# Optimization experiments

Measured on AMD Instinct MI355X. Metric: run time of the kernel, lower is better.

Reference implementation:

```python
import jax, jax.numpy as jnp
import numpy as np

B, S, D, U = 32, 2048, 512, 512

def setup_inputs() -> dict:
    key = jax.random.key(0)
    k1, k2, k3, k4, k5 = jax.random.split(key, 5)
    passage = jax.random.normal(k1, (B, S, D), dtype=jnp.float32)
    hidden = jax.random.normal(k2, (B, D), dtype=jnp.float32)
    mask = jnp.ones((B, S), dtype=jnp.float32)
    # learned params (Dense kernels, glorot-ish scale)
    W1 = jax.random.normal(k3, (D, U), dtype=jnp.float32) / np.sqrt(D)
    W2 = jax.random.normal(k4, (D, U), dtype=jnp.float32) / np.sqrt(D)
    Vw = jax.random.normal(k5, (U, 1), dtype=jnp.float32) / np.sqrt(U)
    Vb = jnp.zeros((1,), dtype=jnp.float32)
    return {"passage": passage, "hidden": hidden, "mask": mask,
            "W1": W1, "W2": W2, "Vw": Vw, "Vb": Vb}

def reference(passage, hidden, mask, W1, W2, Vw, Vb):
    # passage: [B,S,D], hidden: [B,D], mask: [B,S]
    h_proj = jnp.einsum('bd,du->bu', hidden, W2)[:, None, :]        # [B,1,U]
    p_proj = jnp.einsum('bsd,du->bsu', passage, W1)                  # [B,S,U]
    score = jnp.einsum('bsu,uo->bso', jnp.tanh(p_proj + h_proj), Vw) + Vb  # [B,S,1]
    score = score + ((1.0 - mask) * -1e30)[:, :, None]
    attention_weights = jax.nn.softmax(score, axis=1)                # [B,S,1]
    context_vector = jnp.sum(attention_weights * passage, axis=1)    # [B,D]
    return context_vector, attention_weights
```

## Files before the change

### kernel.cpp

```cpp
#include <hip/hip_runtime.h>
#include <hip/hip_bf16.h>
#include <cstddef>


#define NB 32
#define NS 2048
#define ND 512
#define NU 512

typedef __bf16 bf16_t;
typedef __bf16 bf16x8 __attribute__((ext_vector_type(8)));
typedef float floatx4 __attribute__((ext_vector_type(4)));

__global__ __launch_bounds__(256) void prep_kernel(
    const float* __restrict__ W1, bf16_t* __restrict__ W1p,
    const float* __restrict__ hidden, const float* __restrict__ W2,
    float* __restrict__ hproj) {
    if (blockIdx.x < 128) {
        int wave = threadIdx.x >> 6, lane = threadIdx.x & 63;
        int f = (blockIdx.x << 2) + wave;
        int kc = f >> 5, ng = f & 31;
        int q = lane >> 4, c = lane & 15;
        const float* src = W1 + (kc * 32 + q * 8) * 512 + ng * 16 + c;
        bf16x8 w;
#pragma unroll
        for (int jj = 0; jj < 8; ++jj) w[jj] = (bf16_t)src[jj * 512];
        ((bf16x8*)W1p)[(f << 6) + lane] = w;
    } else {
        __shared__ float h[ND];
        __shared__ float part[256];
        int bi = blockIdx.x - 128;
        int b = bi >> 2, ug = bi & 3;
        int t = threadIdx.x;
        h[t] = hidden[b * ND + t];
        h[t + 256] = hidden[b * ND + t + 256];
        __syncthreads();
        int u = (ug << 7) + (t & 127);
        int d0 = (t >> 7) << 8;
        float acc = 0.f;
#pragma unroll 8
        for (int d = d0; d < d0 + 256; ++d) acc = fmaf(h[d], W2[d * NU + u], acc);
        part[t] = acc;
        __syncthreads();
        if (t < 128) hproj[b * NU + u] = part[t] + part[t + 128];
    }
}

__global__ __launch_bounds__(256)
__attribute__((amdgpu_waves_per_eu(2, 2)))
void score_kernel(
    const float* __restrict__ passage, const bf16_t* __restrict__ W1p,
    const float* __restrict__ hproj, const float* __restrict__ Vw,
    const float* __restrict__ Vb, float* __restrict__ scores) {
    __shared__ bf16_t As[64 * 512];
    __shared__ float red[4 * 64];
    const int tid = threadIdx.x;
    const int wave = tid >> 6, lane = tid & 63;
    const int q = lane >> 4, c = lane & 15;
    const int bid = blockIdx.x;
    const int mblk = ((bid >> 4) << 3) + (bid & 7);
    const int nhalf = (bid >> 3) & 1;
    const int m0 = mblk * 64;
    const int b = m0 >> 11;
    const int ng0 = (nhalf << 4) + (wave << 2);
    const bf16x8* Wq = (const bf16x8*)W1p;

#pragma unroll 4
    for (int cc = 0; cc < 16; ++cc) {
        int row = (cc << 2) + wave;
        const float* g = passage + ((size_t)(m0 + row) << 9) + (lane << 3);
        floatx4 f0 = *(const floatx4*)g;
        floatx4 f1 = *(const floatx4*)(g + 4);
        bf16x8 v;
        v[0] = (bf16_t)f0[0]; v[1] = (bf16_t)f0[1];
        v[2] = (bf16_t)f0[2]; v[3] = (bf16_t)f0[3];
        v[4] = (bf16_t)f1[0]; v[5] = (bf16_t)f1[1];
        v[6] = (bf16_t)f1[2]; v[7] = (bf16_t)f1[3];
        unsigned kb = (unsigned)(lane << 4) ^ (unsigned)((row & 7) << 4);
        *(bf16x8*)((char*)As + row * 1024 + kb) = v;
    }

    bf16x8 b_cur[4], b_nxt[4];
#pragma unroll
    for (int j = 0; j < 4; ++j)
        b_cur[j] = Wq[((ng0 + j) << 6) + lane];

    __syncthreads();

    floatx4 acc[4][4];
#pragma unroll
    for (int i = 0; i < 4; ++i)
#pragma unroll
        for (int j = 0; j < 4; ++j) { floatx4 z = {0.f, 0.f, 0.f, 0.f}; acc[i][j] = z; }

    bf16x8 a_cur[4], a_nxt[4];
#pragma unroll
    for (int i = 0; i < 4; ++i) {
        int row = (i << 4) + c;
        unsigned kb = (unsigned)(q << 4) ^ (unsigned)((row & 7) << 4);
        a_cur[i] = *(const bf16x8*)((const char*)As + row * 1024 + kb);
    }

#pragma unroll 2
    for (int kc = 0; kc < 16; ++kc) {
        if (kc < 15) {
#pragma unroll
            for (int j = 0; j < 4; ++j)
                b_nxt[j] = Wq[((((kc + 1) << 5) + ng0 + j) << 6) + lane];
#pragma unroll
            for (int i = 0; i < 4; ++i) {
                int row = (i << 4) + c;
                unsigned kb = (unsigned)(((kc + 1) << 6) + (q << 4)) ^ (unsigned)((row & 7) << 4);
                a_nxt[i] = *(const bf16x8*)((const char*)As + row * 1024 + kb);
            }
        }
        __builtin_amdgcn_s_setprio(1);
#pragma unroll
        for (int i = 0; i < 4; ++i)
#pragma unroll
            for (int j = 0; j < 4; ++j)
                acc[i][j] = __builtin_amdgcn_mfma_f32_16x16x32_bf16(a_cur[i], b_cur[j], acc[i][j], 0, 0, 0);
        __builtin_amdgcn_s_setprio(0);
#pragma unroll
        for (int i = 0; i < 4; ++i) a_cur[i] = a_nxt[i];
#pragma unroll
        for (int j = 0; j < 4; ++j) b_cur[j] = b_nxt[j];
    }

    float sp[4][4];
#pragma unroll
    for (int i = 0; i < 4; ++i)
#pragma unroll
        for (int r = 0; r < 4; ++r) sp[i][r] = 0.f;
#pragma unroll
    for (int j = 0; j < 4; ++j) {
        int n = ((ng0 + j) << 4) + c;
        float hp = hproj[(b << 9) + n];
        float vw = Vw[n];
#pragma unroll
        for (int i = 0; i < 4; ++i)
#pragma unroll
            for (int r = 0; r < 4; ++r) {
                float x = acc[i][j][r] + hp;
                float e = __expf(2.0f * x);
                float t = 1.0f - 2.0f * __builtin_amdgcn_rcpf(e + 1.0f);
                sp[i][r] = fmaf(t, vw, sp[i][r]);
            }
    }
#pragma unroll
    for (int off = 1; off < 16; off <<= 1)
#pragma unroll
        for (int i = 0; i < 4; ++i)
#pragma unroll
            for (int r = 0; r < 4; ++r)
                sp[i][r] += __shfl_xor(sp[i][r], off, 64);

    if (c == 0) {
#pragma unroll
        for (int i = 0; i < 4; ++i)
#pragma unroll
            for (int r = 0; r < 4; ++r)
                red[(wave << 6) + (i << 4) + (q << 2) + r] = sp[i][r];
    }
    __syncthreads();
    if (tid < 64) {
        float s = red[tid] + red[64 + tid] + red[128 + tid] + red[192 + tid];
        if (nhalf == 0) s += Vb[0];
        atomicAdd(&scores[m0 + tid], s);
    }
}

__global__ __launch_bounds__(1024) void softmax_kernel(
    const float* __restrict__ mask, float* __restrict__ attn) {
    __shared__ float smx[16], ssm[16];
    int b = blockIdx.x, tid = threadIdx.x;
    int wave = tid >> 6, lane = tid & 63;
    const int base = b * NS;
    float v0 = attn[base + tid] + (1.0f - mask[base + tid]) * (-1e30f);
    float v1 = attn[base + 1024 + tid] + (1.0f - mask[base + 1024 + tid]) * (-1e30f);
    float mx = fmaxf(v0, v1);
#pragma unroll
    for (int off = 1; off < 64; off <<= 1) mx = fmaxf(mx, __shfl_xor(mx, off, 64));
    if (lane == 0) smx[wave] = mx;
    __syncthreads();
    mx = smx[0];
#pragma unroll
    for (int w = 1; w < 16; ++w) mx = fmaxf(mx, smx[w]);
    v0 = __expf(v0 - mx); v1 = __expf(v1 - mx);
    float sum = v0 + v1;
#pragma unroll
    for (int off = 1; off < 64; off <<= 1) sum += __shfl_xor(sum, off, 64);
    if (lane == 0) ssm[wave] = sum;
    __syncthreads();
    sum = 0.f;
#pragma unroll
    for (int w = 0; w < 16; ++w) sum += ssm[w];
    float inv = 1.0f / sum;
    attn[base + tid] = v0 * inv;
    attn[base + 1024 + tid] = v1 * inv;
}

__global__ __launch_bounds__(512) void context_kernel(
    const float* __restrict__ passage, const float* __restrict__ attn,
    float* __restrict__ ctx) {
    __shared__ float4 part[512];
    int bb = blockIdx.x >> 5, sc = blockIdx.x & 31, t = threadIdx.x;
    int col = t & 127, qh = t >> 7;
    const float4* p = (const float4*)(passage + (((size_t)bb * NS + sc * 64 + qh * 16) << 9));
    const float* wp = attn + bb * NS + sc * 64 + qh * 16;
    float ax = 0.f, ay = 0.f, az = 0.f, aw = 0.f;
#pragma unroll 16
    for (int s = 0; s < 16; ++s) {
        float w = wp[s];
        float4 v = p[(size_t)s * 128 + col];
        ax = fmaf(w, v.x, ax); ay = fmaf(w, v.y, ay);
        az = fmaf(w, v.z, az); aw = fmaf(w, v.w, aw);
    }
    float4 mine; mine.x = ax; mine.y = ay; mine.z = az; mine.w = aw;
    part[t] = mine;
    __syncthreads();
    if (t < 128) {
        float4 o1 = part[t + 128], o2 = part[t + 256], o3 = part[t + 384];
        float* dst = ctx + bb * ND + t * 4;
        atomicAdd(dst + 0, ax + o1.x + o2.x + o3.x);
        atomicAdd(dst + 1, ay + o1.y + o2.y + o3.y);
        atomicAdd(dst + 2, az + o1.z + o2.z + o3.z);
        atomicAdd(dst + 3, aw + o1.w + o2.w + o3.w);
    }
}

extern "C" void kernel_launch(void* const* d_in, const int* in_sizes, int n_in,
                              void* d_out, int out_size, void* d_ws, size_t ws_size,
                              hipStream_t stream) {
    const float* passage = (const float*)d_in[0];
    const float* hidden  = (const float*)d_in[1];
    const float* mask    = (const float*)d_in[2];
    const float* W1      = (const float*)d_in[3];
    const float* W2      = (const float*)d_in[4];
    const float* Vw      = (const float*)d_in[5];
    const float* Vb      = (const float*)d_in[6];

    float* ctx  = (float*)d_out;
    float* attn = (float*)d_out + NB * ND;

    bf16_t* W1p  = (bf16_t*)d_ws;
    float* hproj = (float*)((char*)d_ws + (size_t)NU * ND * 2);

    hipMemsetAsync(ctx, 0, (size_t)NB * (ND + NS) * sizeof(float), stream);
    prep_kernel<<<dim3(256), dim3(256), 0, stream>>>(W1, W1p, hidden, W2, hproj);
    score_kernel<<<dim3(2 * NB * NS / 64), dim3(256), 0, stream>>>(passage, W1p, hproj, Vw, Vb, attn);
    softmax_kernel<<<dim3(NB), dim3(1024), 0, stream>>>(mask, attn);
    context_kernel<<<dim3(NB * 32), dim3(512), 0, stream>>>(passage, attn, ctx);
}
```

Measured before the change: 272.5 us.

## Fuse softmax and context reduction into one finalize kernel

Merges the separate softmax and weighted-sum context kernels into a single finalize kernel. Each block recomputes the per-batch softmax over 2048 scores, keeps the unnormalized exponentials in LDS, and reduces a 32-column slice of passage over the full sequence, so the context is written directly without atomics or a memset of outputs. Scores now go to a workspace buffer and are zeroed there. This removes one launch, the atomics and the attn round-trip, at the cost of 16x redundant softmax work per batch and only 512 blocks with long per-thread sequence loops.

```diff
diff --git a/kernel.cpp b/kernel.cpp
--- a/kernel.cpp
+++ b/kernel.cpp
@@ -170,62 +170,85 @@
     }
 }
 
-__global__ __launch_bounds__(1024) void softmax_kernel(
-    const float* __restrict__ mask, float* __restrict__ attn) {
-    __shared__ float smx[16], ssm[16];
-    int b = blockIdx.x, tid = threadIdx.x;
-    int wave = tid >> 6, lane = tid & 63;
-    const int base = b * NS;
-    float v0 = attn[base + tid] + (1.0f - mask[base + tid]) * (-1e30f);
-    float v1 = attn[base + 1024 + tid] + (1.0f - mask[base + 1024 + tid]) * (-1e30f);
-    float mx = fmaxf(v0, v1);
+__global__ __launch_bounds__(512) void finalize_kernel(
+    const float* __restrict__ passage, const float* __restrict__ scores,
+    const float* __restrict__ mask, float* __restrict__ attn,
+    float* __restrict__ ctx) {
+    __shared__ float wlds[NS];
+    __shared__ float4 part[512];
+    __shared__ float rmx[8], rsm[8];
+    const int b  = blockIdx.x >> 4;
+    const int dc = blockIdx.x & 15;
+    const int t  = threadIdx.x;
+    const int lane = t & 63, wv = t >> 6;
+
+    const float* sc = scores + b * NS;
+    const float* mk = mask + b * NS;
+    float sv[4];
+    float mx = -3.0e38f;
+#pragma unroll
+    for (int i = 0; i < 4; ++i) {
+        int s = t + (i << 9);
+        float v = sc[s] + (1.0f - mk[s]) * (-1e30f);
+        sv[i] = v;
+        mx = fmaxf(mx, v);
+    }
 #pragma unroll
     for (int off = 1; off < 64; off <<= 1) mx = fmaxf(mx, __shfl_xor(mx, off, 64));
-    if (lane == 0) smx[wave] = mx;
-    __syncthreads();
-    mx = smx[0];
-#pragma unroll
-    for (int w = 1; w < 16; ++w) mx = fmaxf(mx, smx[w]);
-    v0 = __expf(v0 - mx); v1 = __expf(v1 - mx);
-    float sum = v0 + v1;
+    if (lane == 0) rmx[wv] = mx;
+    __syncthreads();
+    mx = rmx[0];
+#pragma unroll
+    for (int w = 1; w < 8; ++w) mx = fmaxf(mx, rmx[w]);
+
+    float sum = 0.f;
+#pragma unroll
+    for (int i = 0; i < 4; ++i) {
+        float e = __expf(sv[i] - mx);
+        wlds[t + (i << 9)] = e;
+        sum += e;
+    }
 #pragma unroll
     for (int off = 1; off < 64; off <<= 1) sum += __shfl_xor(sum, off, 64);
-    if (lane == 0) ssm[wave] = sum;
+    if (lane == 0) rsm[wv] = sum;
     __syncthreads();
     sum = 0.f;
 #pragma unroll
-    for (int w = 0; w < 16; ++w) sum += ssm[w];
-    float inv = 1.0f / sum;
-    attn[base + tid] = v0 * inv;
-    attn[base + 1024 + tid] = v1 * inv;
-}
-
-__global__ __launch_bounds__(512) void context_kernel(
-    const float* __restrict__ passage, const float* __restrict__ attn,
-    float* __restrict__ ctx) {
-    __shared__ float4 part[512];
-    int bb = blockIdx.x >> 5, sc = blockIdx.x & 31, t = threadIdx.x;
-    int col = t & 127, qh = t >> 7;
-    const float4* p = (const float4*)(passage + (((size_t)bb * NS + sc * 64 + qh * 16) << 9));
-    const float* wp = attn + bb * NS + sc * 64 + qh * 16;
-    float ax = 0.f, ay = 0.f, az = 0.f, aw = 0.f;
+    for (int w = 0; w < 8; ++w) sum += rsm[w];
+    const float inv = 1.0f / sum;
+
+    const int dq = t & 7;
+    const int sg = t >> 3;
+    const float4* p = (const float4*)(passage + (size_t)b * NS * ND) + dc * 8 + dq;
+    float4 acc; acc.x = acc.y = acc.z = acc.w = 0.f;
+#pragma unroll 8
+    for (int ss = 0; ss < 32; ++ss) {
+        int s = sg + (ss << 6);
+        float w = wlds[s];
+        float4 v = p[(size_t)s * 128];
+        acc.x = fmaf(w, v.x, acc.x); acc.y = fmaf(w, v.y, acc.y);
+        acc.z = fmaf(w, v.z, acc.z); acc.w = fmaf(w, v.w, acc.w);
+    }
+    part[t] = acc;
+    __syncthreads();
+
+    if (t < 8) {
+        float4 a = part[t];
 #pragma unroll 16
-    for (int s = 0; s < 16; ++s) {
-        float w = wp[s];
-        float4 v = p[(size_t)s * 128 + col];
-        ax = fmaf(w, v.x, ax); ay = fmaf(w, v.y, ay);
-        az = fmaf(w, v.z, az); aw = fmaf(w, v.w, aw);
-    }
-    float4 mine; mine.x = ax; mine.y = ay; mine.z = az; mine.w = aw;
-    part[t] = mine;
-    __syncthreads();
-    if (t < 128) {
-        float4 o1 = part[t + 128], o2 = part[t + 256], o3 = part[t + 384];
-        float* dst = ctx + bb * ND + t * 4;
-        atomicAdd(dst + 0, ax + o1.x + o2.x + o3.x);
-        atomicAdd(dst + 1, ay + o1.y + o2.y + o3.y);
-        atomicAdd(dst + 2, az + o1.z + o2.z + o3.z);
-        atomicAdd(dst + 3, aw + o1.w + o2.w + o3.w);
+        for (int g = 1; g < 64; ++g) {
+            float4 o = part[(g << 3) + t];
+            a.x += o.x; a.y += o.y; a.z += o.z; a.w += o.w;
+        }
+        float* dst = ctx + b * ND + dc * 32 + t * 4;
+        dst[0] = a.x * inv; dst[1] = a.y * inv;
+        dst[2] = a.z * inv; dst[3] = a.w * inv;
+    }
+    if (dc == 0) {
+#pragma unroll
+        for (int i = 0; i < 4; ++i) {
+            int s = t + (i << 9);
+            attn[b * NS + s] = wlds[s] * inv;
+        }
     }
 }
 
@@ -243,12 +266,12 @@
     float* ctx  = (float*)d_out;
     float* attn = (float*)d_out + NB * ND;
 
-    bf16_t* W1p  = (bf16_t*)d_ws;
-    float* hproj = (float*)((char*)d_ws + (size_t)NU * ND * 2);
-
-    hipMemsetAsync(ctx, 0, (size_t)NB * (ND + NS) * sizeof(float), stream);
+    bf16_t* W1p   = (bf16_t*)d_ws;
+    float* hproj  = (float*)((char*)d_ws + (size_t)NU * ND * 2);
+    float* scores = (float*)((char*)d_ws + (size_t)NU * ND * 2 + (size_t)NB * NU * 4);
+
+    hipMemsetAsync(scores, 0, (size_t)NB * NS * sizeof(float), stream);
     prep_kernel<<<dim3(256), dim3(256), 0, stream>>>(W1, W1p, hidden, W2, hproj);
-    score_kernel<<<dim3(2 * NB * NS / 64), dim3(256), 0, stream>>>(passage, W1p, hproj, Vw, Vb, attn);
-    softmax_kernel<<<dim3(NB), dim3(1024), 0, stream>>>(mask, attn);
-    context_kernel<<<dim3(NB * 32), dim3(512), 0, stream>>>(passage, attn, ctx);
-}
+    score_kernel<<<dim3(2 * NB * NS / 64), dim3(256), 0, stream>>>(passage, W1p, hproj, Vw, Vb, scores);
+    finalize_kernel<<<dim3(NB * 16), dim3(512), 0, stream>>>(passage, scores, mask, attn, ctx);
+}
```

Measured after the change: 269.8 us. No clear change (-1.0%).
